# Kernel tuning notes

Hardware: AMD Instinct MI355X
Metric: run time of the kernel (lower is better)

The kernel has to match this reference:

```python
import jax, jax.numpy as jnp
import numpy as np

N = 300000   # total atoms
E = 600000   # directed edges
G = 8192     # molecules in batch
D = 6        # node_feat_dim
H = 128      # hidden_dim
OUT = 256    # embedding_dim
L = 4        # num GIN layers


def setup_inputs() -> dict:
    key = jax.random.key(0)
    ks = jax.random.split(key, 12)
    s_in = 1.0 / np.sqrt(D)
    s_h = 1.0 / np.sqrt(H)
    return {
        "x": jax.random.normal(ks[0], (N, D), jnp.float32),
        "edge_index": jax.random.randint(ks[1], (2, E), 0, N, dtype=jnp.int32),
        "batch": jnp.sort(jax.random.randint(ks[2], (N,), 0, G, dtype=jnp.int32)),
        "W_enc": jax.random.normal(ks[3], (D, H), jnp.float32) * s_in,
        "b_enc": jnp.zeros((H,), jnp.float32),
        "W1": jax.random.normal(ks[4], (L, H, H), jnp.float32) * s_h,
        "b1": jnp.zeros((L, H), jnp.float32),
        "W2": jax.random.normal(ks[5], (L, H, H), jnp.float32) * s_h,
        "b2": jnp.zeros((L, H), jnp.float32),
        "W_out": jax.random.normal(ks[6], (H, OUT), jnp.float32) * s_h,
        "b_out": jnp.zeros((OUT,), jnp.float32),
    }


def reference(x, edge_index, batch, W_enc, b_enc, W1, b1, W2, b2, W_out, b_out):
    n = x.shape[0]
    src, dst = edge_index[0], edge_index[1]
    # node encoder
    h = x @ W_enc + b_enc                                   # [N, H]
    # stacked GINConv: out = mlp((1+eps)*x + sum_neighbors), eps = 0
    for l in range(L):
        agg = jax.ops.segment_sum(h[src], dst, num_segments=n)  # gather + scatter-add
        z = h + agg
        z = jax.nn.relu(z @ W1[l] + b1[l]) @ W2[l] + b2[l]      # GIN MLP
        h = jax.nn.relu(z)                                       # outer F.relu
    # global mean pool over graphs
    sums = jax.ops.segment_sum(h, batch, num_segments=G)        # [G, H]
    counts = jax.ops.segment_sum(jnp.ones((n, 1), h.dtype), batch, num_segments=G)
    pooled = sums / jnp.maximum(counts, 1.0)
    return pooled @ W_out + b_out                                # [G, OUT]
```

## Files before the change

### kernel.cpp

```cpp
#include <hip/hip_runtime.h>

#define HD 128

typedef unsigned short ushort_t;
typedef __attribute__((ext_vector_type(8))) unsigned short us8;
typedef __attribute__((ext_vector_type(8))) short s8b;
typedef __attribute__((ext_vector_type(16))) float f32x16;

__device__ __forceinline__ float b2f(unsigned short u) {
    union { unsigned int i; float f; } v; v.i = ((unsigned int)u) << 16; return v.f;
}
__device__ __forceinline__ unsigned short f2b(float f) {
    union { float f; unsigned int i; } v; v.f = f;
    unsigned int u = v.i;
    return (unsigned short)((u + 0x7fffu + ((u >> 16) & 1u)) >> 16);
}

__device__ __forceinline__ void load8f(const float* p, float* o) {
    float4 a = *reinterpret_cast<const float4*>(p);
    float4 b = *reinterpret_cast<const float4*>(p + 4);
    o[0]=a.x;o[1]=a.y;o[2]=a.z;o[3]=a.w;o[4]=b.x;o[5]=b.y;o[6]=b.z;o[7]=b.w;
}
__device__ __forceinline__ void load8b(const ushort_t* p, float* o) {
    us8 v = *reinterpret_cast<const us8*>(p);
#pragma unroll
    for (int j = 0; j < 8; ++j) o[j] = b2f(v[j]);
}
__device__ __forceinline__ void store8b(ushort_t* p, const float* s) {
    us8 v;
#pragma unroll
    for (int j = 0; j < 8; ++j) v[j] = f2b(s[j]);
    *reinterpret_cast<us8*>(p) = v;
}

__device__ __forceinline__ void store1(float* p, float v) { *p = v; }
__device__ __forceinline__ void store1(ushort_t* p, float v) { *p = f2b(v); }

__device__ __forceinline__ int lowerb(const int* __restrict__ a, int n, int v) {
    int lo = 0, hi = n;
    while (lo < hi) { int m = (lo + hi) >> 1; if (a[m] < v) lo = m + 1; else hi = m; }
    return lo;
}

__global__ void hist_kernel(const int* __restrict__ dst, int* __restrict__ deg, int e) {
    int i = blockIdx.x * blockDim.x + threadIdx.x;
    if (i < e) atomicAdd(&deg[dst[i]], 1);
}

#define SCAN_NT 256
#define SCAN_BPT 8
#define SCAN_CHUNK (SCAN_NT * SCAN_BPT)

__global__ __launch_bounds__(SCAN_NT) void scan_a(const int* __restrict__ deg,
                                                  int* __restrict__ bsum, int n) {
    int tid = threadIdx.x;
    int base = blockIdx.x * SCAN_CHUNK + tid * SCAN_BPT;
    int sum = 0;
    if (base + SCAN_BPT <= n) {
        int4 v0 = *reinterpret_cast<const int4*>(deg + base);
        int4 v1 = *reinterpret_cast<const int4*>(deg + base + 4);
        sum = v0.x + v0.y + v0.z + v0.w + v1.x + v1.y + v1.z + v1.w;
    } else {
        for (int j = 0; j < SCAN_BPT; ++j) { int i = base + j; if (i < n) sum += deg[i]; }
    }
    __shared__ int sd[SCAN_NT];
    sd[tid] = sum; __syncthreads();
    for (int off = SCAN_NT / 2; off > 0; off >>= 1) {
        if (tid < off) sd[tid] += sd[tid + off];
        __syncthreads();
    }
    if (tid == 0) bsum[blockIdx.x] = sd[0];
}

__global__ __launch_bounds__(1024) void scan_b(int* __restrict__ bsum, int nb) {
    __shared__ int ps[1024];
    int tid = threadIdx.x;
    int v = (tid < nb) ? bsum[tid] : 0;
    ps[tid] = v; __syncthreads();
    for (int off = 1; off < 1024; off <<= 1) {
        int t = (tid >= off) ? ps[tid - off] : 0;
        __syncthreads();
        ps[tid] += t;
        __syncthreads();
    }
    if (tid < nb) bsum[tid] = ps[tid] - v;
}

__global__ __launch_bounds__(SCAN_NT) void scan_c(const int* __restrict__ deg,
                                                  const int* __restrict__ bsum,
                                                  int* __restrict__ rowptr,
                                                  int* __restrict__ cursor,
                                                  int n, int etot) {
    int tid = threadIdx.x;
    int base = blockIdx.x * SCAN_CHUNK + tid * SCAN_BPT;
    int vals[SCAN_BPT];
    if (base + SCAN_BPT <= n) {
        int4 v0 = *reinterpret_cast<const int4*>(deg + base);
        int4 v1 = *reinterpret_cast<const int4*>(deg + base + 4);
        vals[0]=v0.x; vals[1]=v0.y; vals[2]=v0.z; vals[3]=v0.w;
        vals[4]=v1.x; vals[5]=v1.y; vals[6]=v1.z; vals[7]=v1.w;
    } else {
        for (int j = 0; j < SCAN_BPT; ++j) { int i = base + j; vals[j] = (i < n) ? deg[i] : 0; }
    }
    int sum = 0;
#pragma unroll
    for (int j = 0; j < SCAN_BPT; ++j) sum += vals[j];
    __shared__ int ps[SCAN_NT];
    ps[tid] = sum; __syncthreads();
    for (int off = 1; off < SCAN_NT; off <<= 1) {
        int t = (tid >= off) ? ps[tid - off] : 0;
        __syncthreads();
        ps[tid] += t;
        __syncthreads();
    }
    int run = bsum[blockIdx.x] + ps[tid] - sum;
#pragma unroll
    for (int j = 0; j < SCAN_BPT; ++j) {
        int i = base + j;
        if (i < n) { rowptr[i] = run; cursor[i] = run; run += vals[j]; }
    }
    if (blockIdx.x == 0 && tid == 0) rowptr[n] = etot;
}

__global__ void fill_kernel(const int* __restrict__ src, const int* __restrict__ dst,
                            int* __restrict__ cursor, int* __restrict__ col, int e) {
    int i = blockIdx.x * blockDim.x + threadIdx.x;
    if (i < e) { int slot = atomicAdd(&cursor[dst[i]], 1); col[slot] = src[i]; }
}

__global__ void pack_kernel(const float* __restrict__ W, ushort_t* __restrict__ Wp,
                            int nmat, int ld, int mat_stride, int col_off) {
    int idx = blockIdx.x * blockDim.x + threadIdx.x;
    if (idx >= nmat * 2048) return;
    int lane = idx & 63;
    int ks = (idx >> 6) & 7;
    int j = (idx >> 9) & 3;
    int mat = idx >> 11;
    const float* Wm = W + (size_t)mat * mat_stride;
    int k0 = ks * 16 + (lane >> 5) * 8;
    int n = mat * col_off + j * 32 + (lane & 31);
    us8 o;
#pragma unroll
    for (int e = 0; e < 8; ++e) o[e] = f2b(Wm[(size_t)(k0 + e) * ld + n]);
    *reinterpret_cast<us8*>(Wp + (size_t)idx * 8) = o;
}

__global__ void enc_kernel(const float* __restrict__ x, const float* __restrict__ W,
                           const float* __restrict__ b, ushort_t* __restrict__ h, int n) {
    int idx = blockIdx.x * blockDim.x + threadIdx.x;
    if (idx >= n * 16) return;
    int node = idx >> 4, g = idx & 15;
    const float* xr = x + (size_t)node * 6;
    float xv[6];
#pragma unroll
    for (int d = 0; d < 6; ++d) xv[d] = xr[d];
    float acc[8];
    load8f(b + g * 8, acc);
#pragma unroll
    for (int d = 0; d < 6; ++d) {
        float w[8];
        load8f(W + d * HD + g * 8, w);
#pragma unroll
        for (int j = 0; j < 8; ++j) acc[j] += xv[d] * w[j];
    }
    store8b(h + (size_t)node * HD + g * 8, acc);
}

__global__ void agg_kernel(const ushort_t* __restrict__ h, const int* __restrict__ rowptr,
                           const int* __restrict__ col, ushort_t* __restrict__ z, int n) {
    int t = blockIdx.x * blockDim.x + threadIdx.x;
    int node = t >> 4;
    if (node >= n) return;
    int g = t & 15;
    float acc[8];
    load8b(h + (size_t)node * HD + g * 8, acc);
    int lo = rowptr[node], hi = rowptr[node + 1];
    for (int i = lo; i < hi; ++i) {
        int s = col[i];
        float v[8];
        load8b(h + (size_t)s * HD + g * 8, v);
#pragma unroll
        for (int j = 0; j < 8; ++j) acc[j] += v[j];
    }
    store8b(z + (size_t)node * HD + g * 8, acc);
}

__global__ __launch_bounds__(512) void mlp_fused(
    ushort_t* __restrict__ z,
    const ushort_t* __restrict__ Wp1, const ushort_t* __restrict__ Wp2,
    const float* __restrict__ b1, const float* __restrict__ b2)
{
    __shared__ s8b sW1[2048];
    __shared__ s8b sW2[2048];

    const int tid = threadIdx.x;
    for (int i = tid; i < 2048; i += 512) {
        sW1[i] = reinterpret_cast<const s8b*>(Wp1)[i];
        sW2[i] = reinterpret_cast<const s8b*>(Wp2)[i];
    }
    __syncthreads();

    const int lane = tid & 63;
    const int r32  = lane & 31;
    const int h    = lane >> 5;
    const int row0 = blockIdx.x * 256 + (tid >> 6) * 32;
    const int arow = row0 + r32;
    const int koff = h * 8;

    s8b bz[8];
#pragma unroll
    for (int ks = 0; ks < 8; ++ks)
        bz[ks] = *reinterpret_cast<const s8b*>(z + (size_t)arow * HD + ks * 16 + koff);

    s8b a2[8];
#pragma unroll
    for (int j = 0; j < 4; ++j) {
        f32x16 c;
#pragma unroll
        for (int i = 0; i < 16; ++i) c[i] = 0.f;
#pragma unroll
        for (int ks = 0; ks < 8; ++ks)
            c = __builtin_amdgcn_mfma_f32_32x32x16_bf16(sW1[(j * 8 + ks) * 64 + lane], bz[ks], c, 0, 0, 0);
        unsigned int w[4][2];
#pragma unroll
        for (int b = 0; b < 4; ++b) {
            float4 bv = *reinterpret_cast<const float4*>(b1 + j * 32 + b * 8 + 4 * h);
            float v0 = fmaxf(c[4 * b + 0] + bv.x, 0.f);
            float v1 = fmaxf(c[4 * b + 1] + bv.y, 0.f);
            float v2 = fmaxf(c[4 * b + 2] + bv.z, 0.f);
            float v3 = fmaxf(c[4 * b + 3] + bv.w, 0.f);
            w[b][0] = (unsigned int)f2b(v0) | ((unsigned int)f2b(v1) << 16);
            w[b][1] = (unsigned int)f2b(v2) | ((unsigned int)f2b(v3) << 16);
        }
        unsigned int p[4][2];
#pragma unroll
        for (int b = 0; b < 4; ++b) {
            p[b][0] = (unsigned int)__shfl_xor((int)w[b][0], 32);
            p[b][1] = (unsigned int)__shfl_xor((int)w[b][1], 32);
        }
        union { unsigned int u[4]; s8b v; } t0, t1;
        t0.u[0] = (h == 0) ? w[0][0] : p[1][0];
        t0.u[1] = (h == 0) ? w[0][1] : p[1][1];
        t0.u[2] = (h == 0) ? p[0][0] : w[1][0];
        t0.u[3] = (h == 0) ? p[0][1] : w[1][1];
        t1.u[0] = (h == 0) ? w[2][0] : p[3][0];
        t1.u[1] = (h == 0) ? w[2][1] : p[3][1];
        t1.u[2] = (h == 0) ? p[2][0] : w[3][0];
        t1.u[3] = (h == 0) ? p[2][1] : w[3][1];
        a2[2 * j]     = t0.v;
        a2[2 * j + 1] = t1.v;
    }

#pragma unroll
    for (int j = 0; j < 4; ++j) {
        f32x16 c;
#pragma unroll
        for (int i = 0; i < 16; ++i) c[i] = 0.f;
#pragma unroll
        for (int ks = 0; ks < 8; ++ks)
            c = __builtin_amdgcn_mfma_f32_32x32x16_bf16(a2[ks], sW2[(j * 8 + ks) * 64 + lane], c, 0, 0, 0);
        const int ccol = j * 32 + r32;
        const float bv = b2[ccol];
        const int rbase = row0 + 4 * h;
#pragma unroll
        for (int reg = 0; reg < 16; ++reg) {
            int row = rbase + (reg & 3) + 8 * (reg >> 2);
            z[(size_t)row * HD + ccol] = f2b(fmaxf(c[reg] + bv, 0.f));
        }
    }
}

template<typename TO, bool RELU>
__global__ __launch_bounds__(256) void gemm_mfma(
    const ushort_t* __restrict__ A, const ushort_t* __restrict__ Wp,
    const float* __restrict__ bias, TO* __restrict__ out, int ldo)
{
    __shared__ s8b sW[2048];
    const int tid = threadIdx.x;
    for (int i = tid; i < 2048; i += 256)
        sW[i] = reinterpret_cast<const s8b*>(Wp)[i];
    __syncthreads();

    const int lane = tid & 63;
    const int row0 = blockIdx.x * 128 + (tid >> 6) * 32;
    const int arow = row0 + (lane & 31);
    const int koff = (lane >> 5) * 8;

    s8b a[8];
#pragma unroll
    for (int ks = 0; ks < 8; ++ks)
        a[ks] = *reinterpret_cast<const s8b*>(A + (size_t)arow * HD + ks * 16 + koff);

#pragma unroll
    for (int j = 0; j < 4; ++j) {
        f32x16 acc;
#pragma unroll
        for (int i = 0; i < 16; ++i) acc[i] = 0.f;
#pragma unroll
        for (int ks = 0; ks < 8; ++ks)
            acc = __builtin_amdgcn_mfma_f32_32x32x16_bf16(a[ks], sW[(j * 8 + ks) * 64 + lane], acc, 0, 0, 0);
        const int col = j * 32 + (lane & 31);
        const float bv = bias[col];
        const int rbase = row0 + 4 * (lane >> 5);
#pragma unroll
        for (int reg = 0; reg < 16; ++reg) {
            int row = rbase + (reg & 3) + 8 * (reg >> 2);
            float v = acc[reg] + bv;
            if (RELU) v = fmaxf(v, 0.f);
            store1(out + (size_t)row * ldo + col, v);
        }
    }
}

__global__ __launch_bounds__(128) void pool_kernel(const ushort_t* __restrict__ h,
                                                   const int* __restrict__ batch,
                                                   ushort_t* __restrict__ pooled, int n) {
    int g = blockIdx.x;
    int c = threadIdx.x;
    int start = lowerb(batch, n, g);
    int end = lowerb(batch, n, g + 1);
    float s = 0.f;
    for (int i = start; i < end; ++i) s += b2f(h[(size_t)i * HD + c]);
    int cnt = end - start; if (cnt < 1) cnt = 1;
    pooled[(size_t)g * HD + c] = f2b(s / (float)cnt);
}

extern "C" void kernel_launch(void* const* d_in, const int* in_sizes, int n_in,
                              void* d_out, int out_size, void* d_ws, size_t ws_size,
                              hipStream_t stream) {
    const float* x      = (const float*)d_in[0];
    const int*   edge   = (const int*)d_in[1];
    const int*   batch  = (const int*)d_in[2];
    const float* W_enc  = (const float*)d_in[3];
    const float* b_enc  = (const float*)d_in[4];
    const float* W1     = (const float*)d_in[5];
    const float* b1     = (const float*)d_in[6];
    const float* W2     = (const float*)d_in[7];
    const float* b2     = (const float*)d_in[8];
    const float* W_out  = (const float*)d_in[9];
    const float* b_out  = (const float*)d_in[10];

    const int N = in_sizes[0] / 6;
    const int E = in_sizes[1] / 2;
    const int G = out_size / 256;
    const int L = in_sizes[5] / (HD * HD);
    const int Npad = ((N + 255) / 256) * 256;

    const int* srcv = edge;
    const int* dstv = edge + E;

    size_t off = 0;
    auto alloc = [&](size_t bytes) -> char* {
        char* p = (char*)d_ws + off;
        off += (bytes + 255) & ~(size_t)255;
        return p;
    };
    ushort_t* bufA   = (ushort_t*)alloc((size_t)Npad * HD * 2);
    ushort_t* bufB   = (ushort_t*)alloc((size_t)Npad * HD * 2);
    ushort_t* pooled = (ushort_t*)alloc((size_t)G * HD * 2);
    ushort_t* Wp1    = (ushort_t*)alloc((size_t)L * 16384 * 2);
    ushort_t* Wp2    = (ushort_t*)alloc((size_t)L * 16384 * 2);
    ushort_t* WpO    = (ushort_t*)alloc((size_t)2 * 16384 * 2);
    int* rowptr = (int*)alloc((size_t)(N + 1) * 4);
    int* cursor = (int*)alloc((size_t)N * 4);
    int* colidx = (int*)alloc((size_t)E * 4);
    int* deg    = (int*)alloc((size_t)N * 4);
    int* bsum   = (int*)alloc((size_t)1024 * 4);
    (void)ws_size;

    const int nb = (N + SCAN_CHUNK - 1) / SCAN_CHUNK;
    hipMemsetAsync(deg, 0, (size_t)N * 4, stream);
    hist_kernel<<<(E + 255) / 256, 256, 0, stream>>>(dstv, deg, E);
    scan_a<<<nb, SCAN_NT, 0, stream>>>(deg, bsum, N);
    scan_b<<<1, 1024, 0, stream>>>(bsum, nb);
    scan_c<<<nb, SCAN_NT, 0, stream>>>(deg, bsum, rowptr, cursor, N, E);
    fill_kernel<<<(E + 255) / 256, 256, 0, stream>>>(srcv, dstv, cursor, colidx, E);

    pack_kernel<<<(L * 2048 + 255) / 256, 256, 0, stream>>>(W1, Wp1, L, HD, HD * HD, 0);
    pack_kernel<<<(L * 2048 + 255) / 256, 256, 0, stream>>>(W2, Wp2, L, HD, HD * HD, 0);
    pack_kernel<<<(2 * 2048 + 255) / 256, 256, 0, stream>>>(W_out, WpO, 2, 256, 0, 128);

    enc_kernel<<<(N * 16 + 255) / 256, 256, 0, stream>>>(x, W_enc, b_enc, bufA, N);

    const int nblk = Npad / 256;
    ushort_t* cur = bufA;
    ushort_t* oth = bufB;
    for (int l = 0; l < L; ++l) {
        agg_kernel<<<(N * 16 + 255) / 256, 256, 0, stream>>>(cur, rowptr, colidx, oth, N);
        mlp_fused<<<nblk, 512, 0, stream>>>(
            oth, Wp1 + (size_t)l * 16384, Wp2 + (size_t)l * 16384,
            b1 + (size_t)l * HD, b2 + (size_t)l * HD);
        ushort_t* t = cur; cur = oth; oth = t;
    }

    pool_kernel<<<G, 128, 0, stream>>>(cur, batch, pooled, N);

    float* outp = (float*)d_out;
    gemm_mfma<float, false><<<G / 128, 256, 0, stream>>>(pooled, WpO, b_out, outp, 256);
    gemm_mfma<float, false><<<G / 128, 256, 0, stream>>>(pooled, WpO + 16384, b_out + 128, outp + 128, 256);
}
```

Baseline: 523.8 us.

## Aggregate raw 6-dim features before encoder to skip first-layer 128-dim gather

The node encoder is linear, so the first layer's neighbor sum of encoded features equals the encoder applied to the summed raw inputs plus degree-scaled bias. The first aggregation now gathers only 6 floats per neighbor instead of 128 bf16 values, then applies the encoder once per node to produce z directly. This removes one full 128-wide gather pass and adds a small intermediate buffer. It also hints the MLP kernel with a minimum-occupancy launch bound, and rounding differs slightly because the sum is done in fp32 before encoding.

```diff
diff --git a/kernel.cpp b/kernel.cpp
--- a/kernel.cpp
+++ b/kernel.cpp
@@ -145,25 +145,53 @@
     *reinterpret_cast<us8*>(Wp + (size_t)idx * 8) = o;
 }
 
-__global__ void enc_kernel(const float* __restrict__ x, const float* __restrict__ W,
-                           const float* __restrict__ b, ushort_t* __restrict__ h, int n) {
-    int idx = blockIdx.x * blockDim.x + threadIdx.x;
-    if (idx >= n * 16) return;
-    int node = idx >> 4, g = idx & 15;
-    const float* xr = x + (size_t)node * 6;
-    float xv[6];
-#pragma unroll
-    for (int d = 0; d < 6; ++d) xv[d] = xr[d];
-    float acc[8];
-    load8f(b + g * 8, acc);
-#pragma unroll
-    for (int d = 0; d < 6; ++d) {
-        float w[8];
-        load8f(W + d * HD + g * 8, w);
-#pragma unroll
-        for (int j = 0; j < 8; ++j) acc[j] += xv[d] * w[j];
-    }
-    store8b(h + (size_t)node * HD + g * 8, acc);
+__global__ void xagg_kernel(const float* __restrict__ x, const int* __restrict__ rowptr,
+                            const int* __restrict__ col, float* __restrict__ xa, int n) {
+    int node = blockIdx.x * blockDim.x + threadIdx.x;
+    if (node >= n) return;
+    const float2* xr = reinterpret_cast<const float2*>(x + (size_t)node * 6);
+    float2 a0 = xr[0], a1 = xr[1], a2 = xr[2];
+    int lo = rowptr[node], hi = rowptr[node + 1];
+    for (int i = lo; i < hi; ++i) {
+        const float2* xs = reinterpret_cast<const float2*>(x + (size_t)col[i] * 6);
+        float2 s0 = xs[0], s1 = xs[1], s2 = xs[2];
+        a0.x += s0.x; a0.y += s0.y; a1.x += s1.x; a1.y += s1.y; a2.x += s2.x; a2.y += s2.y;
+    }
+    float cnt = (float)(1 + hi - lo);
+    float4 o0; o0.x = a0.x; o0.y = a0.y; o0.z = a1.x; o0.w = a1.y;
+    float4 o1; o1.x = a2.x; o1.y = a2.y; o1.z = cnt; o1.w = 0.f;
+    reinterpret_cast<float4*>(xa + (size_t)node * 8)[0] = o0;
+    reinterpret_cast<float4*>(xa + (size_t)node * 8)[1] = o1;
+}
+
+__global__ void enc2_kernel(const float* __restrict__ xa, const float* __restrict__ W,
+                            const float* __restrict__ b, ushort_t* __restrict__ z, int n) {
+    int t = blockIdx.x * blockDim.x + threadIdx.x;
+    int q = t >> 4, g = t & 15;
+    int node0 = q * 4;
+    if (node0 >= n) return;
+    float w[6][8];
+#pragma unroll
+    for (int d = 0; d < 6; ++d) load8f(W + d * HD + g * 8, w[d]);
+    float bias[8];
+    load8f(b + g * 8, bias);
+#pragma unroll
+    for (int u = 0; u < 4; ++u) {
+        int node = node0 + u;
+        if (node >= n) break;
+        float4 a0 = reinterpret_cast<const float4*>(xa + (size_t)node * 8)[0];
+        float4 a1 = reinterpret_cast<const float4*>(xa + (size_t)node * 8)[1];
+        float xv[6] = {a0.x, a0.y, a0.z, a0.w, a1.x, a1.y};
+        float cnt = a1.z;
+        float acc[8];
+#pragma unroll
+        for (int j = 0; j < 8; ++j) acc[j] = cnt * bias[j];
+#pragma unroll
+        for (int d = 0; d < 6; ++d)
+#pragma unroll
+            for (int j = 0; j < 8; ++j) acc[j] += xv[d] * w[d][j];
+        store8b(z + (size_t)node * HD + g * 8, acc);
+    }
 }
 
 __global__ void agg_kernel(const ushort_t* __restrict__ h, const int* __restrict__ rowptr,
@@ -185,7 +213,7 @@
     store8b(z + (size_t)node * HD + g * 8, acc);
 }
 
-__global__ __launch_bounds__(512) void mlp_fused(
+__global__ __launch_bounds__(512, 4) void mlp_fused(
     ushort_t* __restrict__ z,
     const ushort_t* __restrict__ Wp1, const ushort_t* __restrict__ Wp2,
     const float* __restrict__ b1, const float* __restrict__ b2)
@@ -361,6 +389,7 @@
     ushort_t* Wp1    = (ushort_t*)alloc((size_t)L * 16384 * 2);
     ushort_t* Wp2    = (ushort_t*)alloc((size_t)L * 16384 * 2);
     ushort_t* WpO    = (ushort_t*)alloc((size_t)2 * 16384 * 2);
+    float* xaggb = (float*)alloc((size_t)N * 8 * 4);
     int* rowptr = (int*)alloc((size_t)(N + 1) * 4);
     int* cursor = (int*)alloc((size_t)N * 4);
     int* colidx = (int*)alloc((size_t)E * 4);
@@ -380,12 +409,17 @@
     pack_kernel<<<(L * 2048 + 255) / 256, 256, 0, stream>>>(W2, Wp2, L, HD, HD * HD, 0);
     pack_kernel<<<(2 * 2048 + 255) / 256, 256, 0, stream>>>(W_out, WpO, 2, 256, 0, 128);
 
-    enc_kernel<<<(N * 16 + 255) / 256, 256, 0, stream>>>(x, W_enc, b_enc, bufA, N);
-
+    xagg_kernel<<<(N + 255) / 256, 256, 0, stream>>>(x, rowptr, colidx, xaggb, N);
+    {
+        int threads = ((N + 3) / 4) * 16;
+        enc2_kernel<<<(threads + 255) / 256, 256, 0, stream>>>(xaggb, W_enc, b_enc, bufA, N);
+    }
     const int nblk = Npad / 256;
+    mlp_fused<<<nblk, 512, 0, stream>>>(bufA, Wp1, Wp2, b1, b2);
+
     ushort_t* cur = bufA;
     ushort_t* oth = bufB;
-    for (int l = 0; l < L; ++l) {
+    for (int l = 1; l < L; ++l) {
         agg_kernel<<<(N * 16 + 255) / 256, 256, 0, stream>>>(cur, rowptr, colidx, oth, N);
         mlp_fused<<<nblk, 512, 0, stream>>>(
             oth, Wp1 + (size_t)l * 16384, Wp2 + (size_t)l * 16384,
```

New measurement: 466.8 us. -10.9%, faster.
